# Optimization experiments

Hardware: AMD Instinct MI355X
Metric: run time of the kernel (lower is better)

The kernel has to match this reference:

```python
import jax, jax.numpy as jnp
import numpy as np

N_NODES = 100000
N_EDGES = 1600000
NFEAT, NHID, NCLASS = 256, 512, 256


def _init_params(key):
    ks = jax.random.split(key, 8)
    s = 0.02
    p = {
        'W1a': jax.random.normal(ks[0], (NFEAT, NHID), jnp.float32) * s,
        'b1a': jnp.zeros((NHID,), jnp.float32),
        'W1b': jax.random.normal(ks[1], (NHID, NHID), jnp.float32) * s,
        'b1b': jnp.zeros((NHID,), jnp.float32),
        'W2a': jax.random.normal(ks[2], (NHID, NHID), jnp.float32) * s,
        'b2a': jnp.zeros((NHID,), jnp.float32),
        'W2b': jax.random.normal(ks[3], (NHID, NCLASS), jnp.float32) * s,
        'b2b': jnp.zeros((NCLASS,), jnp.float32),
        'eps1': jnp.zeros((), jnp.float32),
        'eps2': jnp.zeros((), jnp.float32),
    }
    return p


def setup_inputs() -> dict:
    key = jax.random.key(0)
    kx, ke, kp = jax.random.split(key, 3)
    x = jax.random.normal(kx, (N_NODES, NFEAT), jnp.float32)
    edge_index = jax.random.randint(ke, (2, N_EDGES), 0, N_NODES, jnp.int64)
    inp = {'x': x, 'edge_index': edge_index}
    inp.update(_init_params(kp))
    return inp


def _gin_agg(h, src, dst, eps, n_nodes):
    # sum of neighbor (source) features at each destination node + (1+eps)*self
    agg = jax.ops.segment_sum(h[src], dst, num_segments=n_nodes)
    return (1.0 + eps) * h + agg


def reference(x, edge_index, W1a, b1a, W1b, b1b, W2a, b2a, W2b, b2b, eps1, eps2):
    src, dst = edge_index[0], edge_index[1]
    n = x.shape[0]
    # GINConv layer 1: MLP = Linear-ReLU-Linear-ReLU
    h = _gin_agg(x, src, dst, eps1, n)
    h = jax.nn.relu(h @ W1a + b1a)
    h = jax.nn.relu(h @ W1b + b1b)
    # dropout: eval mode (identity)
    # GINConv layer 2: MLP = Linear-ReLU-Linear
    h = _gin_agg(h, src, dst, eps2, n)
    h = jax.nn.relu(h @ W2a + b2a)
    out = h @ W2b + b2b
    return out
```

## Files before the change

### kernel.cpp

```cpp
#include <hip/hip_runtime.h>
#include <hip/hip_bf16.h>
#include <stdint.h>

#define NN 100000
#define NFEATD 256
#define NHIDD 512
#define NCLASSD 256

typedef short bf16x8 __attribute__((ext_vector_type(8)));
typedef float f32x4 __attribute__((ext_vector_type(4)));
typedef float f32x2 __attribute__((ext_vector_type(2)));

__device__ __forceinline__ float bf2f(uint32_t u) {
    union { uint32_t i; float f; } v; v.i = u << 16; return v.f;
}
__device__ __forceinline__ ushort f2bf(float f) {
    uint32_t x = __float_as_uint(f);
    uint32_t r = (x + 0x7FFF + ((x >> 16) & 1)) >> 16;
    return (ushort)r;
}

__global__ void zero_i32(int* __restrict__ p, int n) {
    int i = blockIdx.x * 256 + threadIdx.x;
    if (i < n) p[i] = 0;
}

__global__ void count_deg(const int* __restrict__ dst, int* __restrict__ deg, int nE) {
    int e = blockIdx.x * 256 + threadIdx.x;
    if (e < nE) atomicAdd(&deg[dst[e]], 1);
}

__global__ __launch_bounds__(1024) void scan_excl(const int* __restrict__ deg,
                                                  int* __restrict__ off, int n) {
    __shared__ int wsum[16];
    __shared__ int carry_s;
    const int tid = threadIdx.x;
    const int lane = tid & 63, wv = tid >> 6;
    if (tid == 0) carry_s = 0;
    __syncthreads();
    for (int base = 0; base < n; base += 1024) {
        int i = base + tid;
        int v = (i < n) ? deg[i] : 0;
        int x = v;
#pragma unroll
        for (int d = 1; d < 64; d <<= 1) {
            int y = __shfl_up(x, d, 64);
            if (lane >= d) x += y;
        }
        if (lane == 63) wsum[wv] = x;
        __syncthreads();
        if (wv == 0 && lane < 16) {
            int s = wsum[lane];
#pragma unroll
            for (int d = 1; d < 16; d <<= 1) {
                int y = __shfl_up(s, d, 16);
                if (lane >= d) s += y;
            }
            wsum[lane] = s;
        }
        __syncthreads();
        int carry = carry_s;
        int wprefix = (wv == 0) ? 0 : wsum[wv - 1];
        if (i < n) off[i] = carry + wprefix + x - v;
        __syncthreads();
        if (tid == 0) carry_s = carry + wsum[15];
        __syncthreads();
    }
    if (tid == 0) off[n] = carry_s;
}

__global__ void fill_csr(const int* __restrict__ src, const int* __restrict__ dst,
                         const int* __restrict__ off, int* __restrict__ cursor,
                         int* __restrict__ csr, int nE) {
    int e = blockIdx.x * 256 + threadIdx.x;
    if (e >= nE) return;
    int d = dst[e];
    int p = off[d] + atomicAdd(&cursor[d], 1);
    csr[p] = src[e];
}

__global__ void prep_w4(const float* __restrict__ W1a, const float* __restrict__ W1b,
                        const float* __restrict__ W2a, const float* __restrict__ W2b,
                        ushort* __restrict__ Wt1a, ushort* __restrict__ Wt1b,
                        ushort* __restrict__ Wt2a, ushort* __restrict__ Wt2b) {
    int idx = blockIdx.x * 256 + threadIdx.x;
    if (idx < 131072) {
        int k = idx >> 9, n = idx & 511;
        Wt1a[n * 256 + k] = f2bf(W1a[idx]);
    } else if (idx < 131072 + 262144) {
        int i = idx - 131072;
        int k = i >> 9, n = i & 511;
        Wt1b[n * 512 + k] = f2bf(W1b[i]);
    } else if (idx < 131072 + 524288) {
        int i = idx - (131072 + 262144);
        int k = i >> 9, n = i & 511;
        Wt2a[n * 512 + k] = f2bf(W2a[i]);
    } else if (idx < 131072 + 524288 + 131072) {
        int i = idx - (131072 + 524288);
        int k = i >> 8, n = i & 255;
        Wt2b[n * 512 + k] = f2bf(W2b[i]);
    }
}

__global__ void cast_f32_fp8(const float* __restrict__ a, uint8_t* __restrict__ o, int n) {
    int i = (blockIdx.x * 256 + threadIdx.x) * 8;
    if (i >= n) return;
    float4 v0 = *(const float4*)(a + i);
    float4 v1 = *(const float4*)(a + i + 4);
    int lo = __builtin_amdgcn_cvt_pk_fp8_f32(v0.x, v0.y, 0, false);
    lo = __builtin_amdgcn_cvt_pk_fp8_f32(v0.z, v0.w, lo, true);
    int hi = __builtin_amdgcn_cvt_pk_fp8_f32(v1.x, v1.y, 0, false);
    hi = __builtin_amdgcn_cvt_pk_fp8_f32(v1.z, v1.w, hi, true);
    uint2 r; r.x = (uint32_t)lo; r.y = (uint32_t)hi;
    *(uint2*)(o + i) = r;
}

__device__ __forceinline__ void accp(uint32_t p, f32x2& lo, f32x2& hi) {
    lo += __builtin_amdgcn_cvt_pk_f32_fp8((int)p, false);
    hi += __builtin_amdgcn_cvt_pk_f32_fp8((int)p, true);
}

__global__ void gather256f8(const uint8_t* __restrict__ X8, const int* __restrict__ off,
                            const int* __restrict__ csr, const float* __restrict__ eps,
                            ushort* __restrict__ out) {
    int node = (blockIdx.x * 256 + threadIdx.x) >> 6;
    if (node >= NN) return;
    int lane = threadIdx.x & 63;
    float sc = 1.0f + *eps;
    f32x2 scv = {sc, sc};
    const uint32_t* X1 = (const uint32_t*)X8;
    f32x2 lo = {0.f, 0.f}, hi = {0.f, 0.f};
    {
        uint32_t p = X1[(size_t)node * 64 + lane];
        lo = scv * __builtin_amdgcn_cvt_pk_f32_fp8((int)p, false);
        hi = scv * __builtin_amdgcn_cvt_pk_f32_fp8((int)p, true);
    }
    int e = off[node], e1 = off[node + 1];
    for (; e + 7 < e1; e += 8) {
        uint32_t p[8];
#pragma unroll
        for (int t = 0; t < 8; ++t) p[t] = X1[(size_t)csr[e + t] * 64 + lane];
#pragma unroll
        for (int t = 0; t < 8; ++t) accp(p[t], lo, hi);
    }
    for (; e < e1; ++e)
        accp(X1[(size_t)csr[e] * 64 + lane], lo, hi);
    uint2 r;
    r.x = (uint32_t)f2bf(lo[0]) | ((uint32_t)f2bf(lo[1]) << 16);
    r.y = (uint32_t)f2bf(hi[0]) | ((uint32_t)f2bf(hi[1]) << 16);
    *(uint2*)(out + (size_t)node * 256 + lane * 4) = r;
}

__global__ void gather512f8(const uint8_t* __restrict__ H8, const int* __restrict__ off,
                            const int* __restrict__ csr, const float* __restrict__ eps,
                            ushort* __restrict__ out) {
    int node = (blockIdx.x * 256 + threadIdx.x) >> 6;
    if (node >= NN) return;
    int lane = threadIdx.x & 63;
    float sc = 1.0f + *eps;
    f32x2 scv = {sc, sc};
    const uint2* H2 = (const uint2*)H8;
    f32x2 l0 = {0.f, 0.f}, h0 = {0.f, 0.f}, l1 = {0.f, 0.f}, h1 = {0.f, 0.f};
    {
        uint2 p = H2[(size_t)node * 64 + lane];
        l0 = scv * __builtin_amdgcn_cvt_pk_f32_fp8((int)p.x, false);
        h0 = scv * __builtin_amdgcn_cvt_pk_f32_fp8((int)p.x, true);
        l1 = scv * __builtin_amdgcn_cvt_pk_f32_fp8((int)p.y, false);
        h1 = scv * __builtin_amdgcn_cvt_pk_f32_fp8((int)p.y, true);
    }
    int e = off[node], e1 = off[node + 1];
    for (; e + 7 < e1; e += 8) {
        uint2 p[8];
#pragma unroll
        for (int t = 0; t < 8; ++t) p[t] = H2[(size_t)csr[e + t] * 64 + lane];
#pragma unroll
        for (int t = 0; t < 8; ++t) {
            accp(p[t].x, l0, h0);
            accp(p[t].y, l1, h1);
        }
    }
    for (; e < e1; ++e) {
        uint2 p = H2[(size_t)csr[e] * 64 + lane];
        accp(p.x, l0, h0);
        accp(p.y, l1, h1);
    }
    uint4 r;
    r.x = (uint32_t)f2bf(l0[0]) | ((uint32_t)f2bf(l0[1]) << 16);
    r.y = (uint32_t)f2bf(h0[0]) | ((uint32_t)f2bf(h0[1]) << 16);
    r.z = (uint32_t)f2bf(l1[0]) | ((uint32_t)f2bf(l1[1]) << 16);
    r.w = (uint32_t)f2bf(h1[0]) | ((uint32_t)f2bf(h1[1]) << 16);
    *(uint4*)(out + (size_t)node * 512 + lane * 8) = r;
}

__global__ __launch_bounds__(256) void gemm_bt(
    const ushort* __restrict__ A, const ushort* __restrict__ Bt,
    const float* __restrict__ bias, float* __restrict__ outf,
    uint8_t* __restrict__ out8, ushort* __restrict__ outb,
    int M, int N, int K, int relu)
{
    __shared__ ushort As[128 * 32];
    __shared__ ushort Bs[128 * 32];
    const int tid = threadIdx.x;
    const int wave = tid >> 6, lane = tid & 63;
    const int quad = lane >> 4, lrow = lane & 15;
    const int wr = wave >> 1, wc = wave & 1;
    const int row0 = blockIdx.y * 128, col0 = blockIdx.x * 128;

    f32x4 acc[4][4] = {};

    for (int k0 = 0; k0 < K; k0 += 32) {
#pragma unroll
        for (int it = 0; it < 2; ++it) {
            int chunk = it * 256 + tid;
            int r = chunk >> 2, c = chunk & 3;
            int gr = row0 + r; if (gr > M - 1) gr = M - 1;
            const ushort* gp = A + (size_t)gr * K + (k0 + c * 8);
            __builtin_amdgcn_global_load_lds((const __attribute__((address_space(1))) void*)gp,
                (__attribute__((address_space(3))) void*)(As + chunk * 8), 16, 0, 0);
        }
#pragma unroll
        for (int it = 0; it < 2; ++it) {
            int chunk = it * 256 + tid;
            int r = chunk >> 2, c = chunk & 3;
            const ushort* gp = Bt + (size_t)(col0 + r) * K + (k0 + c * 8);
            __builtin_amdgcn_global_load_lds((const __attribute__((address_space(1))) void*)gp,
                (__attribute__((address_space(3))) void*)(Bs + chunk * 8), 16, 0, 0);
        }
        __syncthreads();

        bf16x8 af[4], bfr[4];
#pragma unroll
        for (int i = 0; i < 4; ++i)
            af[i] = *(const bf16x8*)(As + (wr * 64 + i * 16 + lrow) * 32 + quad * 8);
#pragma unroll
        for (int j = 0; j < 4; ++j)
            bfr[j] = *(const bf16x8*)(Bs + (wc * 64 + j * 16 + lrow) * 32 + quad * 8);
#pragma unroll
        for (int i = 0; i < 4; ++i)
#pragma unroll
            for (int j = 0; j < 4; ++j)
                acc[i][j] = __builtin_amdgcn_mfma_f32_16x16x32_bf16(bfr[j], af[i], acc[i][j], 0, 0, 0);
        __syncthreads();
    }

#pragma unroll
    for (int i = 0; i < 4; ++i) {
        int rr = row0 + wr * 64 + i * 16 + lrow;
        if (rr < M) {
#pragma unroll
            for (int j = 0; j < 4; ++j) {
                int c = col0 + wc * 64 + j * 16 + quad * 4;
                float4 bv = *(const float4*)(bias + c);
                float v0 = acc[i][j][0] + bv.x;
                float v1 = acc[i][j][1] + bv.y;
                float v2 = acc[i][j][2] + bv.z;
                float v3 = acc[i][j][3] + bv.w;
                if (relu) {
                    v0 = fmaxf(v0, 0.f); v1 = fmaxf(v1, 0.f);
                    v2 = fmaxf(v2, 0.f); v3 = fmaxf(v3, 0.f);
                }
                if (outf) {
                    float4 o; o.x = v0; o.y = v1; o.z = v2; o.w = v3;
                    *(float4*)(outf + (size_t)rr * N + c) = o;
                } else if (out8) {
                    int enc = __builtin_amdgcn_cvt_pk_fp8_f32(v0, v1, 0, false);
                    enc = __builtin_amdgcn_cvt_pk_fp8_f32(v2, v3, enc, true);
                    *(uint32_t*)(out8 + (size_t)rr * N + c) = (uint32_t)enc;
                } else {
                    uint2 o;
                    o.x = (uint32_t)f2bf(v0) | ((uint32_t)f2bf(v1) << 16);
                    o.y = (uint32_t)f2bf(v2) | ((uint32_t)f2bf(v3) << 16);
                    *(uint2*)(outb + (size_t)rr * N + c) = o;
                }
            }
        }
    }
}

extern "C" void kernel_launch(void* const* d_in, const int* in_sizes, int n_in,
                              void* d_out, int out_size, void* d_ws, size_t ws_size,
                              hipStream_t stream) {
    const float* x    = (const float*)d_in[0];
    const int*   ei   = (const int*)d_in[1];
    const float* W1a  = (const float*)d_in[2];
    const float* b1a  = (const float*)d_in[3];
    const float* W1b  = (const float*)d_in[4];
    const float* b1b  = (const float*)d_in[5];
    const float* W2a  = (const float*)d_in[6];
    const float* b2a  = (const float*)d_in[7];
    const float* W2b  = (const float*)d_in[8];
    const float* b2b  = (const float*)d_in[9];
    const float* eps1 = (const float*)d_in[10];
    const float* eps2 = (const float*)d_in[11];
    const int nE = in_sizes[1] / 2;
    const int* srcv = ei;
    const int* dstv = ei + nE;

    char* ws = (char*)d_ws;
    int*    off    = (int*)(ws);
    int*    cursor = (int*)(ws + 524288);
    int*    csr    = (int*)(ws + 1048576);
    ushort* Wt1a   = (ushort*)(ws + 8388608);
    ushort* Wt1b   = Wt1a + 512 * 256;
    ushort* Wt2a   = Wt1b + 512 * 512;
    ushort* Wt2b   = Wt2a + 512 * 512;
    char*   P      = ws + 10485760;
    char*   Q      = ws + 10485760 + 102400000;
    uint8_t* x8    = (uint8_t*)P;
    ushort* agg1b  = (ushort*)Q;
    ushort* h1     = (ushort*)P;
    uint8_t* h2f8  = (uint8_t*)Q;
    ushort* agg2b  = (ushort*)P;
    ushort* h3     = (ushort*)Q;

    zero_i32<<<(NN + 255) / 256, 256, 0, stream>>>(cursor, NN);
    count_deg<<<(nE + 255) / 256, 256, 0, stream>>>(dstv, cursor, nE);
    scan_excl<<<1, 1024, 0, stream>>>(cursor, off, NN);
    zero_i32<<<(NN + 255) / 256, 256, 0, stream>>>(cursor, NN);
    fill_csr<<<(nE + 255) / 256, 256, 0, stream>>>(srcv, dstv, off, cursor, csr, nE);

    prep_w4<<<(786432 + 255) / 256, 256, 0, stream>>>(W1a, W1b, W2a, W2b,
                                                      Wt1a, Wt1b, Wt2a, Wt2b);
    cast_f32_fp8<<<(NN * NFEATD / 8 + 255) / 256, 256, 0, stream>>>(x, x8, NN * NFEATD);

    gather256f8<<<(NN * 64) / 256, 256, 0, stream>>>(x8, off, csr, eps1, agg1b);
    dim3 g1(NHIDD / 128, (NN + 127) / 128);
    gemm_bt<<<g1, 256, 0, stream>>>(agg1b, Wt1a, b1a, nullptr, nullptr, h1, NN, NHIDD, NFEATD, 1);
    gemm_bt<<<g1, 256, 0, stream>>>(h1, Wt1b, b1b, nullptr, h2f8, nullptr, NN, NHIDD, NHIDD, 1);

    gather512f8<<<(NN * 64) / 256, 256, 0, stream>>>(h2f8, off, csr, eps2, agg2b);
    gemm_bt<<<g1, 256, 0, stream>>>(agg2b, Wt2a, b2a, nullptr, nullptr, h3, NN, NHIDD, NHIDD, 1);
    dim3 g2(NCLASSD / 128, (NN + 127) / 128);
    gemm_bt<<<g2, 256, 0, stream>>>(h3, Wt2b, b2b, (float*)d_out, nullptr, nullptr, NN, NCLASSD, NHIDD, 0);
}
```

Before: 987.5 us.

## Double-buffer GEMM LDS tiles and widen blocks to 128x256 with 8 waves

The GEMM now uses a two-stage LDS ping-pong buffer: the next K-chunk is issued via global_load_lds while MFMAs run on the current one, which removes one barrier per iteration. Block tiles grow from 128x128 to 128x256 with 512 threads (8 waves), so each A tile is reused across twice as many columns. MFMA sections are wrapped in s_setprio. Per-block LDS use grows to 48KB and launch bounds request 4 blocks per CU, which may limit occupancy.

```diff
diff --git a/kernel.cpp b/kernel.cpp
--- a/kernel.cpp
+++ b/kernel.cpp
@@ -192,69 +192,84 @@
     *(uint4*)(out + (size_t)node * 512 + lane * 8) = r;
 }
 
-__global__ __launch_bounds__(256) void gemm_bt(
+
+__device__ __forceinline__ void stage_a(const ushort* __restrict__ A, int K, int row0,
+                                        int kc, ushort* dst, int tid, int Mm1) {
+    int r = tid >> 2, c = tid & 3;
+    int gr = row0 + r; if (gr > Mm1) gr = Mm1;
+    const ushort* gp = A + (size_t)gr * K + kc + c * 8;
+    __builtin_amdgcn_global_load_lds((const __attribute__((address_space(1))) void*)gp,
+        (__attribute__((address_space(3))) void*)(dst + tid * 8), 16, 0, 0);
+}
+
+__device__ __forceinline__ void stage_b(const ushort* __restrict__ Bt, int K, int col0,
+                                        int kc, ushort* dst, int tid) {
+#pragma unroll
+    for (int i = 0; i < 2; ++i) {
+        int u = i * 512 + tid;
+        int r = u >> 2, c = u & 3;
+        const ushort* gp = Bt + (size_t)(col0 + r) * K + kc + c * 8;
+        __builtin_amdgcn_global_load_lds((const __attribute__((address_space(1))) void*)gp,
+            (__attribute__((address_space(3))) void*)(dst + u * 8), 16, 0, 0);
+    }
+}
+
+__global__ __launch_bounds__(512, 4) void gemm_bt(
     const ushort* __restrict__ A, const ushort* __restrict__ Bt,
     const float* __restrict__ bias, float* __restrict__ outf,
     uint8_t* __restrict__ out8, ushort* __restrict__ outb,
     int M, int N, int K, int relu)
 {
-    __shared__ ushort As[128 * 32];
-    __shared__ ushort Bs[128 * 32];
+    __shared__ ushort smem[2][12288];
     const int tid = threadIdx.x;
     const int wave = tid >> 6, lane = tid & 63;
     const int quad = lane >> 4, lrow = lane & 15;
-    const int wr = wave >> 1, wc = wave & 1;
-    const int row0 = blockIdx.y * 128, col0 = blockIdx.x * 128;
+    const int wr = wave >> 2, wcn = wave & 3;
+    const int row0 = blockIdx.y * 128, col0 = blockIdx.x * 256;
+    const int NC = K >> 5;
 
     f32x4 acc[4][4] = {};
 
-    for (int k0 = 0; k0 < K; k0 += 32) {
-#pragma unroll
-        for (int it = 0; it < 2; ++it) {
-            int chunk = it * 256 + tid;
-            int r = chunk >> 2, c = chunk & 3;
-            int gr = row0 + r; if (gr > M - 1) gr = M - 1;
-            const ushort* gp = A + (size_t)gr * K + (k0 + c * 8);
-            __builtin_amdgcn_global_load_lds((const __attribute__((address_space(1))) void*)gp,
-                (__attribute__((address_space(3))) void*)(As + chunk * 8), 16, 0, 0);
-        }
-#pragma unroll
-        for (int it = 0; it < 2; ++it) {
-            int chunk = it * 256 + tid;
-            int r = chunk >> 2, c = chunk & 3;
-            const ushort* gp = Bt + (size_t)(col0 + r) * K + (k0 + c * 8);
-            __builtin_amdgcn_global_load_lds((const __attribute__((address_space(1))) void*)gp,
-                (__attribute__((address_space(3))) void*)(Bs + chunk * 8), 16, 0, 0);
-        }
-        __syncthreads();
-
+    stage_a(A, K, row0, 0, smem[0], tid, M - 1);
+    stage_b(Bt, K, col0, 0, smem[0] + 4096, tid);
+    __syncthreads();
+
+    for (int t = 0; t < NC; ++t) {
+        const ushort* As = smem[t & 1];
+        const ushort* Bs = As + 4096;
+        if (t + 1 < NC) {
+            stage_a(A, K, row0, (t + 1) << 5, smem[(t + 1) & 1], tid, M - 1);
+            stage_b(Bt, K, col0, (t + 1) << 5, smem[(t + 1) & 1] + 4096, tid);
+        }
         bf16x8 af[4], bfr[4];
 #pragma unroll
-        for (int i = 0; i < 4; ++i)
-            af[i] = *(const bf16x8*)(As + (wr * 64 + i * 16 + lrow) * 32 + quad * 8);
-#pragma unroll
-        for (int j = 0; j < 4; ++j)
-            bfr[j] = *(const bf16x8*)(Bs + (wc * 64 + j * 16 + lrow) * 32 + quad * 8);
-#pragma unroll
-        for (int i = 0; i < 4; ++i)
-#pragma unroll
-            for (int j = 0; j < 4; ++j)
-                acc[i][j] = __builtin_amdgcn_mfma_f32_16x16x32_bf16(bfr[j], af[i], acc[i][j], 0, 0, 0);
-        __syncthreads();
-    }
-
-#pragma unroll
-    for (int i = 0; i < 4; ++i) {
-        int rr = row0 + wr * 64 + i * 16 + lrow;
+        for (int m = 0; m < 4; ++m)
+            af[m] = *(const bf16x8*)(As + (wr * 64 + m * 16 + lrow) * 32 + quad * 8);
+#pragma unroll
+        for (int n = 0; n < 4; ++n)
+            bfr[n] = *(const bf16x8*)(Bs + (wcn * 64 + n * 16 + lrow) * 32 + quad * 8);
+        __builtin_amdgcn_s_setprio(1);
+#pragma unroll
+        for (int m = 0; m < 4; ++m)
+#pragma unroll
+            for (int n = 0; n < 4; ++n)
+                acc[m][n] = __builtin_amdgcn_mfma_f32_16x16x32_bf16(bfr[n], af[m], acc[m][n], 0, 0, 0);
+        __builtin_amdgcn_s_setprio(0);
+        __syncthreads();
+    }
+
+#pragma unroll
+    for (int m = 0; m < 4; ++m) {
+        int rr = row0 + wr * 64 + m * 16 + lrow;
         if (rr < M) {
 #pragma unroll
-            for (int j = 0; j < 4; ++j) {
-                int c = col0 + wc * 64 + j * 16 + quad * 4;
+            for (int n = 0; n < 4; ++n) {
+                int c = col0 + wcn * 64 + n * 16 + quad * 4;
                 float4 bv = *(const float4*)(bias + c);
-                float v0 = acc[i][j][0] + bv.x;
-                float v1 = acc[i][j][1] + bv.y;
-                float v2 = acc[i][j][2] + bv.z;
-                float v3 = acc[i][j][3] + bv.w;
+                float v0 = acc[m][n][0] + bv.x;
+                float v1 = acc[m][n][1] + bv.y;
+                float v2 = acc[m][n][2] + bv.z;
+                float v3 = acc[m][n][3] + bv.w;
                 if (relu) {
                     v0 = fmaxf(v0, 0.f); v1 = fmaxf(v1, 0.f);
                     v2 = fmaxf(v2, 0.f); v3 = fmaxf(v3, 0.f);
@@ -324,12 +339,12 @@
     cast_f32_fp8<<<(NN * NFEATD / 8 + 255) / 256, 256, 0, stream>>>(x, x8, NN * NFEATD);
 
     gather256f8<<<(NN * 64) / 256, 256, 0, stream>>>(x8, off, csr, eps1, agg1b);
-    dim3 g1(NHIDD / 128, (NN + 127) / 128);
-    gemm_bt<<<g1, 256, 0, stream>>>(agg1b, Wt1a, b1a, nullptr, nullptr, h1, NN, NHIDD, NFEATD, 1);
-    gemm_bt<<<g1, 256, 0, stream>>>(h1, Wt1b, b1b, nullptr, h2f8, nullptr, NN, NHIDD, NHIDD, 1);
+    dim3 g1(NHIDD / 256, (NN + 127) / 128);
+    gemm_bt<<<g1, 512, 0, stream>>>(agg1b, Wt1a, b1a, nullptr, nullptr, h1, NN, NHIDD, NFEATD, 1);
+    gemm_bt<<<g1, 512, 0, stream>>>(h1, Wt1b, b1b, nullptr, h2f8, nullptr, NN, NHIDD, NHIDD, 1);
 
     gather512f8<<<(NN * 64) / 256, 256, 0, stream>>>(h2f8, off, csr, eps2, agg2b);
-    gemm_bt<<<g1, 256, 0, stream>>>(agg2b, Wt2a, b2a, nullptr, nullptr, h3, NN, NHIDD, NHIDD, 1);
-    dim3 g2(NCLASSD / 128, (NN + 127) / 128);
-    gemm_bt<<<g2, 256, 0, stream>>>(h3, Wt2b, b2b, (float*)d_out, nullptr, nullptr, NN, NCLASSD, NHIDD, 0);
-}
+    gemm_bt<<<g1, 512, 0, stream>>>(agg2b, Wt2a, b2a, nullptr, nullptr, h3, NN, NHIDD, NHIDD, 1);
+    dim3 g2(NCLASSD / 256, (NN + 127) / 128);
+    gemm_bt<<<g2, 512, 0, stream>>>(h3, Wt2b, b2b, (float*)d_out, nullptr, nullptr, NN, NCLASSD, NHIDD, 0);
+}
```

Result: faster. 927.4 us (-6.1%).
